# Kernel tuning notes

Measured on AMD Instinct MI355X. Metric: run time of the kernel, lower is better.

## Reference

```python
import jax, jax.numpy as jnp
import numpy as np

N, D = 2097152, 10  # tokens, feature dim (pinned by nn.Linear(10,10))


def setup_inputs() -> dict:
    key = jax.random.key(0)
    kx, kr, kw1, kb1, kw2, kb2 = jax.random.split(key, 6)
    s = 1.0 / np.sqrt(D)  # torch nn.Linear default init range
    x = jax.random.normal(kx, (N, D), dtype=jnp.float32)
    route = jax.random.randint(kr, (N,), 0, 2, dtype=jnp.int32)  # RandScatter decision
    W1 = jax.random.uniform(kw1, (D, D), jnp.float32, -s, s)
    b1 = jax.random.uniform(kb1, (D,), jnp.float32, -s, s)
    W2 = jax.random.uniform(kw2, (D, D), jnp.float32, -s, s)
    b2 = jax.random.uniform(kb2, (D,), jnp.float32, -s, s)
    return {"x": x, "W1": W1, "b1": b1, "W2": W2, "b2": b2, "route": route}


def reference(x, W1, b1, W2, b2, route):
    # Original: scatter rows by `route` to expert1/expert2 (Linear 10->10),
    # then gather back to original row order. Equivalent dense form:
    # out[i] = expert_{route[i]}(x[i]). The 10x10 GEMMs are negligible, so
    # computing both branches and selecting is the efficient vectorized form.
    y0 = x @ W1.T + b1  # [N, D] expert1 on all rows
    y1 = x @ W2.T + b2  # [N, D] expert2 on all rows
    return jnp.where((route == 0)[:, None], y0, y1)
```

## Files before the change

### kernel.cpp

```cpp
#include <hip/hip_runtime.h>


#define BLOCK 256
#define D 10
#define ROWS_PER_WAVE 128
#define ROWS_PER_BLOCK 512
#define F4_PER_WAVE 320

__global__ __launch_bounds__(BLOCK) void moe_kernel(
    const float* __restrict__ x,
    const float* __restrict__ W1,
    const float* __restrict__ b1,
    const float* __restrict__ W2,
    const float* __restrict__ b2,
    const int*   __restrict__ route,
    float*       __restrict__ out,
    int n)
{
    __shared__ float4 lds[(BLOCK / 64) * F4_PER_WAVE];

    const int lane = threadIdx.x & 63;
    const int wave = threadIdx.x >> 6;
    const long long rowbase =
        ((long long)blockIdx.x * (BLOCK / 64) + wave) * ROWS_PER_WAVE;

    float4* __restrict__ wlds = lds + wave * F4_PER_WAVE;

    if (rowbase + ROWS_PER_WAVE <= n) {
        const float4* __restrict__ xv = (const float4*)(x + rowbase * D);
        float4*       __restrict__ ov = (float4*)(out + rowbase * D);

        #pragma unroll
        for (int j = 0; j < 5; ++j)
            wlds[j * 64 + lane] = xv[j * 64 + lane];

        const int2 rt = ((const int2*)(route + rowbase))[lane];
        const int rsel[2] = {rt.x, rt.y};

        __builtin_amdgcn_wave_barrier();

        float4 xr[5];
        #pragma unroll
        for (int j = 0; j < 5; ++j)
            xr[j] = wlds[lane * 5 + j];

        float xf[2 * D];
        #pragma unroll
        for (int j = 0; j < 5; ++j) {
            xf[4 * j + 0] = xr[j].x; xf[4 * j + 1] = xr[j].y;
            xf[4 * j + 2] = xr[j].z; xf[4 * j + 3] = xr[j].w;
        }

        float yf[2 * D];
        #pragma unroll
        for (int r = 0; r < 2; ++r) {
            #pragma unroll
            for (int j = 0; j < D; ++j) {
                float y0 = b1[j];
                float y1 = b2[j];
                #pragma unroll
                for (int k = 0; k < D; ++k) {
                    const float xk = xf[r * D + k];
                    y0 = fmaf(xk, W1[j * D + k], y0);
                    y1 = fmaf(xk, W2[j * D + k], y1);
                }
                yf[r * D + j] = rsel[r] ? y1 : y0;
            }
        }

        #pragma unroll
        for (int j = 0; j < 5; ++j) {
            float4 t;
            t.x = yf[4 * j + 0]; t.y = yf[4 * j + 1];
            t.z = yf[4 * j + 2]; t.w = yf[4 * j + 3];
            wlds[lane * 5 + j] = t;
        }

        __builtin_amdgcn_wave_barrier();

        #pragma unroll
        for (int j = 0; j < 5; ++j)
            ov[j * 64 + lane] = wlds[j * 64 + lane];
    } else {
        for (int r = 0; r < 2; ++r) {
            const long long row = rowbase + lane * 2 + r;
            if (row < n) {
                const int sel = route[row];
                for (int j = 0; j < D; ++j) {
                    float y0 = b1[j];
                    float y1 = b2[j];
                    for (int k = 0; k < D; ++k) {
                        const float xk = x[row * D + k];
                        y0 = fmaf(xk, W1[j * D + k], y0);
                        y1 = fmaf(xk, W2[j * D + k], y1);
                    }
                    out[row * D + j] = sel ? y1 : y0;
                }
            }
        }
    }
}

extern "C" void kernel_launch(void* const* d_in, const int* in_sizes, int n_in,
                              void* d_out, int out_size, void* d_ws, size_t ws_size,
                              hipStream_t stream) {
    const float* x     = (const float*)d_in[0];
    const float* W1    = (const float*)d_in[1];
    const float* b1    = (const float*)d_in[2];
    const float* W2    = (const float*)d_in[3];
    const float* b2    = (const float*)d_in[4];
    const int*   route = (const int*)d_in[5];
    float*       out   = (float*)d_out;

    const int n = in_sizes[5];
    const int blocks = (n + ROWS_PER_BLOCK - 1) / ROWS_PER_BLOCK;

    moe_kernel<<<blocks, BLOCK, 0, stream>>>(x, W1, b1, W2, b2, route, out, n);
}
```

Before: 165.5 us.

## Process four chunks per block with register double-buffered prefetch and nontemporal stores

Each block now handles four 512-row chunks, prefetching the next chunk's x and route into registers while the current chunk is computed and staged through LDS. Output writes use nontemporal stores, and launch bounds request 4 blocks per CU. The aim is to overlap global load latency with compute and cut per-block launch overhead in this memory-bound kernel. In exchange, registers per thread go up and the grid has a quarter as many blocks, so fewer waves are available to hide latency.

```diff
diff --git a/kernel.cpp b/kernel.cpp
--- a/kernel.cpp
+++ b/kernel.cpp
@@ -3,11 +3,14 @@
 
 #define BLOCK 256
 #define D 10
-#define ROWS_PER_WAVE 128
-#define ROWS_PER_BLOCK 512
+#define WAVE_ROWS 128
 #define F4_PER_WAVE 320
+#define BLK_ROWS (4 * WAVE_ROWS)
+#define ITERS 4
 
-__global__ __launch_bounds__(BLOCK) void moe_kernel(
+typedef float f4 __attribute__((ext_vector_type(4)));
+
+__global__ __launch_bounds__(BLOCK, 4) void moe_kernel(
     const float* __restrict__ x,
     const float* __restrict__ W1,
     const float* __restrict__ b1,
@@ -17,40 +20,45 @@
     float*       __restrict__ out,
     int n)
 {
-    __shared__ float4 lds[(BLOCK / 64) * F4_PER_WAVE];
+    __shared__ f4 lds[(BLOCK / 64) * F4_PER_WAVE];
 
     const int lane = threadIdx.x & 63;
     const int wave = threadIdx.x >> 6;
-    const long long rowbase =
-        ((long long)blockIdx.x * (BLOCK / 64) + wave) * ROWS_PER_WAVE;
+    f4* __restrict__ wlds = lds + wave * F4_PER_WAVE;
 
-    float4* __restrict__ wlds = lds + wave * F4_PER_WAVE;
+    const long long blkbase = (long long)blockIdx.x * (BLK_ROWS * ITERS);
 
-    if (rowbase + ROWS_PER_WAVE <= n) {
-        const float4* __restrict__ xv = (const float4*)(x + rowbase * D);
-        float4*       __restrict__ ov = (float4*)(out + rowbase * D);
+    auto wave_rowbase = [&](int it) -> long long {
+        return blkbase + (long long)it * BLK_ROWS + (long long)wave * WAVE_ROWS;
+    };
+
+    auto load_chunk = [&](int it, f4* bx, int2& br) {
+        const long long rb = wave_rowbase(it);
+        const f4* __restrict__ xv = (const f4*)(x + rb * D);
+        #pragma unroll
+        for (int j = 0; j < 5; ++j)
+            bx[j] = xv[j * 64 + lane];
+        br = ((const int2*)(route + rb))[lane];
+    };
+
+    auto process_chunk = [&](int it, const f4* bx, int2 br) {
+        const long long rb = wave_rowbase(it);
+        f4* __restrict__ ov = (f4*)(out + rb * D);
 
         #pragma unroll
         for (int j = 0; j < 5; ++j)
-            wlds[j * 64 + lane] = xv[j * 64 + lane];
-
-        const int2 rt = ((const int2*)(route + rowbase))[lane];
-        const int rsel[2] = {rt.x, rt.y};
-
+            wlds[j * 64 + lane] = bx[j];
         __builtin_amdgcn_wave_barrier();
-
-        float4 xr[5];
-        #pragma unroll
-        for (int j = 0; j < 5; ++j)
-            xr[j] = wlds[lane * 5 + j];
 
         float xf[2 * D];
         #pragma unroll
         for (int j = 0; j < 5; ++j) {
-            xf[4 * j + 0] = xr[j].x; xf[4 * j + 1] = xr[j].y;
-            xf[4 * j + 2] = xr[j].z; xf[4 * j + 3] = xr[j].w;
+            f4 t = wlds[lane * 5 + j];
+            xf[4 * j + 0] = t.x; xf[4 * j + 1] = t.y;
+            xf[4 * j + 2] = t.z; xf[4 * j + 3] = t.w;
         }
 
+        const int rsel[2] = {br.x, br.y};
         float yf[2 * D];
         #pragma unroll
         for (int r = 0; r < 2; ++r) {
@@ -70,31 +78,47 @@
 
         #pragma unroll
         for (int j = 0; j < 5; ++j) {
-            float4 t;
+            f4 t;
             t.x = yf[4 * j + 0]; t.y = yf[4 * j + 1];
             t.z = yf[4 * j + 2]; t.w = yf[4 * j + 3];
             wlds[lane * 5 + j] = t;
         }
-
         __builtin_amdgcn_wave_barrier();
 
         #pragma unroll
-        for (int j = 0; j < 5; ++j)
-            ov[j * 64 + lane] = wlds[j * 64 + lane];
+        for (int j = 0; j < 5; ++j) {
+            f4 t = wlds[j * 64 + lane];
+            __builtin_nontemporal_store(t, &ov[j * 64 + lane]);
+        }
+        __builtin_amdgcn_wave_barrier();
+    };
+
+    if (blkbase + (long long)ITERS * BLK_ROWS <= n) {
+        f4   buf[2][5];
+        int2 brt[2];
+        load_chunk(0, buf[0], brt[0]);
+        #pragma unroll
+        for (int it = 0; it < ITERS; ++it) {
+            if (it + 1 < ITERS)
+                load_chunk(it + 1, buf[(it + 1) & 1], brt[(it + 1) & 1]);
+            process_chunk(it, buf[it & 1], brt[it & 1]);
+        }
     } else {
-        for (int r = 0; r < 2; ++r) {
-            const long long row = rowbase + lane * 2 + r;
-            if (row < n) {
-                const int sel = route[row];
-                for (int j = 0; j < D; ++j) {
-                    float y0 = b1[j];
-                    float y1 = b2[j];
-                    for (int k = 0; k < D; ++k) {
-                        const float xk = x[row * D + k];
-                        y0 = fmaf(xk, W1[j * D + k], y0);
-                        y1 = fmaf(xk, W2[j * D + k], y1);
+        for (int it = 0; it < ITERS; ++it) {
+            for (int r = 0; r < 2; ++r) {
+                const long long row = wave_rowbase(it) + lane * 2 + r;
+                if (row < n) {
+                    const int sel = route[row];
+                    for (int j = 0; j < D; ++j) {
+                        float y0 = b1[j];
+                        float y1 = b2[j];
+                        for (int k = 0; k < D; ++k) {
+                            const float xk = x[row * D + k];
+                            y0 = fmaf(xk, W1[j * D + k], y0);
+                            y1 = fmaf(xk, W2[j * D + k], y1);
+                        }
+                        out[row * D + j] = sel ? y1 : y0;
                     }
-                    out[row * D + j] = sel ? y1 : y0;
                 }
             }
         }
@@ -113,7 +137,8 @@
     float*       out   = (float*)d_out;
 
     const int n = in_sizes[5];
-    const int blocks = (n + ROWS_PER_BLOCK - 1) / ROWS_PER_BLOCK;
+    const int rows_per_block = BLK_ROWS * ITERS;
+    const int blocks = (n + rows_per_block - 1) / rows_per_block;
 
     moe_kernel<<<blocks, BLOCK, 0, stream>>>(x, W1, b1, W2, b2, route, out, n);
 }
```

Result: slower. 172.1 us (+4.0%).

## Pack two rows into float2 FMAs and store outputs directly with nontemporal writes

Applied to the files above, without the earlier changes.

Rows are now processed in pairs with float2 vector FMAs so the compiler can emit packed FMA instructions. The LDS round-trip on the output side is removed: each lane writes its five float4 outputs straight to global memory with nontemporal stores, which leaves adjacent lanes writing strided 80-byte chunks instead of coalesced float4s. Input loads are now staged through registers before going into LDS. The aim is to cut LDS traffic and ALU count in this bandwidth-bound kernel, at the risk of less efficient write coalescing.

```diff
diff --git a/kernel.cpp b/kernel.cpp
--- a/kernel.cpp
+++ b/kernel.cpp
@@ -3,9 +3,12 @@
 
 #define BLOCK 256
 #define D 10
-#define ROWS_PER_WAVE 128
+#define WAVE_ROWS 128
+#define F4_PER_WAVE 320
 #define ROWS_PER_BLOCK 512
-#define F4_PER_WAVE 320
+
+typedef float f4 __attribute__((ext_vector_type(4)));
+typedef float f2 __attribute__((ext_vector_type(2)));
 
 __global__ __launch_bounds__(BLOCK) void moe_kernel(
     const float* __restrict__ x,
@@ -17,70 +20,68 @@
     float*       __restrict__ out,
     int n)
 {
-    __shared__ float4 lds[(BLOCK / 64) * F4_PER_WAVE];
+    __shared__ f4 lds[(BLOCK / 64) * F4_PER_WAVE];
 
     const int lane = threadIdx.x & 63;
     const int wave = threadIdx.x >> 6;
+    f4* __restrict__ wlds = lds + wave * F4_PER_WAVE;
+
     const long long rowbase =
-        ((long long)blockIdx.x * (BLOCK / 64) + wave) * ROWS_PER_WAVE;
+        ((long long)blockIdx.x * (BLOCK / 64) + wave) * WAVE_ROWS;
 
-    float4* __restrict__ wlds = lds + wave * F4_PER_WAVE;
-
-    if (rowbase + ROWS_PER_WAVE <= n) {
-        const float4* __restrict__ xv = (const float4*)(x + rowbase * D);
-        float4*       __restrict__ ov = (float4*)(out + rowbase * D);
+    if (rowbase + WAVE_ROWS <= n) {
+        const f4* __restrict__ xv = (const f4*)(x + rowbase * D);
+        f4 bx[5];
+        #pragma unroll
+        for (int j = 0; j < 5; ++j)
+            bx[j] = xv[j * 64 + lane];
+        const int2 rt = ((const int2*)(route + rowbase))[lane];
 
         #pragma unroll
         for (int j = 0; j < 5; ++j)
-            wlds[j * 64 + lane] = xv[j * 64 + lane];
-
-        const int2 rt = ((const int2*)(route + rowbase))[lane];
-        const int rsel[2] = {rt.x, rt.y};
-
+            wlds[j * 64 + lane] = bx[j];
         __builtin_amdgcn_wave_barrier();
-
-        float4 xr[5];
-        #pragma unroll
-        for (int j = 0; j < 5; ++j)
-            xr[j] = wlds[lane * 5 + j];
 
         float xf[2 * D];
         #pragma unroll
         for (int j = 0; j < 5; ++j) {
-            xf[4 * j + 0] = xr[j].x; xf[4 * j + 1] = xr[j].y;
-            xf[4 * j + 2] = xr[j].z; xf[4 * j + 3] = xr[j].w;
+            f4 t = wlds[lane * 5 + j];
+            xf[4 * j + 0] = t.x; xf[4 * j + 1] = t.y;
+            xf[4 * j + 2] = t.z; xf[4 * j + 3] = t.w;
         }
 
-        float yf[2 * D];
+        f2 xp[D];
         #pragma unroll
-        for (int r = 0; r < 2; ++r) {
+        for (int k = 0; k < D; ++k)
+            xp[k] = (f2){xf[k], xf[D + k]};
+
+        float o0[D], o1[D];
+        #pragma unroll
+        for (int j = 0; j < D; ++j) {
+            f2 a0 = (f2){b1[j], b1[j]};
+            f2 a1 = (f2){b2[j], b2[j]};
             #pragma unroll
-            for (int j = 0; j < D; ++j) {
-                float y0 = b1[j];
-                float y1 = b2[j];
-                #pragma unroll
-                for (int k = 0; k < D; ++k) {
-                    const float xk = xf[r * D + k];
-                    y0 = fmaf(xk, W1[j * D + k], y0);
-                    y1 = fmaf(xk, W2[j * D + k], y1);
-                }
-                yf[r * D + j] = rsel[r] ? y1 : y0;
+            for (int k = 0; k < D; ++k) {
+                const float w1 = W1[j * D + k];
+                const float w2 = W2[j * D + k];
+                a0 = __builtin_elementwise_fma(xp[k], (f2){w1, w1}, a0);
+                a1 = __builtin_elementwise_fma(xp[k], (f2){w2, w2}, a1);
             }
+            o0[j] = rt.x ? a1.x : a0.x;
+            o1[j] = rt.y ? a1.y : a0.y;
         }
 
-        #pragma unroll
-        for (int j = 0; j < 5; ++j) {
-            float4 t;
-            t.x = yf[4 * j + 0]; t.y = yf[4 * j + 1];
-            t.z = yf[4 * j + 2]; t.w = yf[4 * j + 3];
-            wlds[lane * 5 + j] = t;
-        }
-
-        __builtin_amdgcn_wave_barrier();
-
-        #pragma unroll
-        for (int j = 0; j < 5; ++j)
-            ov[j * 64 + lane] = wlds[j * 64 + lane];
+        f4* __restrict__ ov = (f4*)(out + rowbase * D) + lane * 5;
+        f4 t0 = (f4){o0[0], o0[1], o0[2], o0[3]};
+        f4 t1 = (f4){o0[4], o0[5], o0[6], o0[7]};
+        f4 t2 = (f4){o0[8], o0[9], o1[0], o1[1]};
+        f4 t3 = (f4){o1[2], o1[3], o1[4], o1[5]};
+        f4 t4 = (f4){o1[6], o1[7], o1[8], o1[9]};
+        __builtin_nontemporal_store(t0, ov + 0);
+        __builtin_nontemporal_store(t1, ov + 1);
+        __builtin_nontemporal_store(t2, ov + 2);
+        __builtin_nontemporal_store(t3, ov + 3);
+        __builtin_nontemporal_store(t4, ov + 4);
     } else {
         for (int r = 0; r < 2; ++r) {
             const long long row = rowbase + lane * 2 + r;
```

Result: slower. 233.2 us (+40.9%).
